# Kernel tuning notes

Measured on AMD Instinct MI355X. Metric: run time of the kernel, lower is better.

## Reference

```python
import jax, jax.numpy as jnp
import numpy as np

N_TOKENS = 100000
N_ARGS = 20000
N_EDGES = 320000
IN_DIM = 768
HEADS = 8
OUT_DIM = 64


def setup_inputs() -> dict:
    key = jax.random.key(0)
    k1, k2, k3, k4, k5 = jax.random.split(key, 5)
    h = jax.random.normal(k1, (N_TOKENS, IN_DIM), dtype=jnp.float32)
    W_fc = jax.random.normal(k2, (HEADS * OUT_DIM, IN_DIM), dtype=jnp.float32) * 0.05
    a_attn = jax.random.normal(k3, (2 * OUT_DIM,), dtype=jnp.float32) * 0.1
    edge_src = jax.random.randint(k4, (N_EDGES,), 0, N_TOKENS, dtype=jnp.int32)
    edge_dst = jax.random.randint(k5, (N_EDGES,), 0, N_ARGS, dtype=jnp.int32)
    return {"h": h, "W_fc": W_fc, "a_attn": a_attn,
            "edge_src": edge_src, "edge_dst": edge_dst}


def reference(h, W_fc, a_attn, edge_src, edge_dst):
    # z = fc(h) reshaped to [N_TOKENS, HEADS, OUT_DIM]
    z = (h @ W_fc.T).reshape(N_TOKENS, HEADS, OUT_DIM)
    # DGL zero-initializes 'z' on arg (dst) nodes, so the dst half of attn_fc
    # contributes 0; only the src half of the attention vector matters.
    a_src = a_attn[:OUT_DIM]
    s_node = jnp.einsum('nhd,d->nh', z, a_src)            # [N_TOKENS, H]
    e = jax.nn.leaky_relu(s_node[edge_src])               # [E, H]
    # segment softmax over incoming edges of each arg node
    m = jax.ops.segment_max(e, edge_dst, num_segments=N_ARGS)   # [N_ARGS, H]
    ex = jnp.exp(e - m[edge_dst])                          # [E, H]
    denom = jax.ops.segment_sum(ex, edge_dst, num_segments=N_ARGS)
    denom = jnp.where(denom == 0, 1.0, denom)
    alpha = ex / denom[edge_dst]                           # [E, H]
    # weighted neighbor aggregation
    msg = alpha[:, :, None] * z[edge_src]                  # [E, H, D]
    out = jax.ops.segment_sum(msg, edge_dst, num_segments=N_ARGS)  # [N_ARGS, H, D]
    return out
```

## Files before the change

kernel.cpp:

```cpp
#include <hip/hip_runtime.h>
#include <hip/hip_bf16.h>
#include <stdint.h>

#define N_TOKENS 100000
#define N_ARGS   20000
#define N_EDGES  320000
#define IN_DIM   768
#define HEADS    8
#define OUT_DIM  64
#define ZDIM     512

typedef unsigned short u16;
typedef unsigned int   u32;
typedef __bf16 bf16x8 __attribute__((ext_vector_type(8)));
typedef float  f32x4  __attribute__((ext_vector_type(4)));

__device__ __forceinline__ u16 f2bf(float f) {
    union { float f; u32 i; } v; v.f = f;
    u32 u = v.i;
    u += 0x7fffu + ((u >> 16) & 1u);
    return (u16)(u >> 16);
}
__device__ __forceinline__ float bf2f(u16 u) {
    union { u32 i; float f; } v; v.i = ((u32)u) << 16; return v.f;
}
__device__ __forceinline__ u32 pk(float lo, float hi) {
    __hip_bfloat162 r = __float22bfloat162_rn(float2{lo, hi});
    union { __hip_bfloat162 b; u32 u; } v; v.b = r; return v.u;
}
__device__ __forceinline__ uint4 pack8(const float4 p, const float4 q) {
    uint4 w;
    w.x = pk(p.x, p.y); w.y = pk(p.z, p.w);
    w.z = pk(q.x, q.y); w.w = pk(q.z, q.w);
    return w;
}

__global__ __launch_bounds__(256) void gemm_kernel(
    const float* __restrict__ A,
    const float* __restrict__ B,
    const float* __restrict__ a_attn,
    u16* __restrict__ z,
    float* __restrict__ s_node)
{
    __shared__ u16 As[128 * 32];
    __shared__ u16 Bs[128 * 32];

    const int tid  = threadIdx.x;
    const int wave = tid >> 6, lane = tid & 63;
    const int quad = lane >> 4, l16 = lane & 15;
    const int wm = wave >> 1, wn = wave & 1;
    const int bx = blockIdx.x;
    const int tileN = bx & 3;
    const int tileM = bx >> 2;

    const int tr = tid >> 1;
    const int tc = (tid & 1) * 16;
    int ga_row = tileM * 128 + tr; if (ga_row >= N_TOKENS) ga_row = N_TOKENS - 1;
    const float* gA = A + (size_t)ga_row * IN_DIM + tc;
    const float* gB = B + (size_t)(tileN * 128 + tr) * IN_DIM + tc;
    u16* sA = As + tid * 16;
    u16* sB = Bs + tid * 16;

    f32x4 acc[4][4];
    const f32x4 zero4 = {0.f, 0.f, 0.f, 0.f};
#pragma unroll
    for (int i = 0; i < 4; i++)
#pragma unroll
        for (int j = 0; j < 4; j++) acc[i][j] = zero4;

    for (int kt = 0; kt < IN_DIM / 32; ++kt) {
        const float4* pa = reinterpret_cast<const float4*>(gA + kt * 32);
        const float4* pb = reinterpret_cast<const float4*>(gB + kt * 32);
        const float4 a0 = pa[0], a1 = pa[1], a2 = pa[2], a3 = pa[3];
        const float4 b0 = pb[0], b1 = pb[1], b2 = pb[2], b3 = pb[3];
        __syncthreads();
        reinterpret_cast<uint4*>(sA)[0] = pack8(a0, a1);
        reinterpret_cast<uint4*>(sA)[1] = pack8(a2, a3);
        reinterpret_cast<uint4*>(sB)[0] = pack8(b0, b1);
        reinterpret_cast<uint4*>(sB)[1] = pack8(b2, b3);
        __syncthreads();

        bf16x8 aF[4], bF[4];
#pragma unroll
        for (int i = 0; i < 4; i++)
            aF[i] = *reinterpret_cast<const bf16x8*>(As + (wm * 64 + i * 16 + l16) * 32 + quad * 8);
#pragma unroll
        for (int j = 0; j < 4; j++)
            bF[j] = *reinterpret_cast<const bf16x8*>(Bs + (wn * 64 + j * 16 + l16) * 32 + quad * 8);
#pragma unroll
        for (int i = 0; i < 4; i++)
#pragma unroll
            for (int j = 0; j < 4; j++)
                acc[i][j] = __builtin_amdgcn_mfma_f32_16x16x32_bf16(aF[i], bF[j], acc[i][j], 0, 0, 0);
    }

    float av[4];
#pragma unroll
    for (int j = 0; j < 4; j++) av[j] = a_attn[j * 16 + l16];
    const int head = tileN * 2 + wn;
    const int colb = tileN * 128 + wn * 64;
#pragma unroll
    for (int i = 0; i < 4; i++) {
        const int rowb = tileM * 128 + wm * 64 + i * 16 + quad * 4;
#pragma unroll
        for (int r = 0; r < 4; r++) {
            const int row = rowb + r;
            const bool ok = row < N_TOKENS;
            float p = 0.0f;
#pragma unroll
            for (int j = 0; j < 4; j++) {
                const float v = acc[i][j][r];
                p += v * av[j];
                if (ok) z[(size_t)row * ZDIM + colb + j * 16 + l16] = f2bf(v);
            }
            p += __shfl_xor(p, 1);
            p += __shfl_xor(p, 2);
            p += __shfl_xor(p, 4);
            p += __shfl_xor(p, 8);
            if (ok && l16 == 0) s_node[row * HEADS + head] = p;
        }
    }
}

__global__ void zero_kernel(int* __restrict__ p, int n) {
    int i = blockIdx.x * blockDim.x + threadIdx.x;
    if (i < n) p[i] = 0;
}

__global__ void hist_kernel(const int* __restrict__ edst, int* __restrict__ counts) {
    int i = blockIdx.x * blockDim.x + threadIdx.x;
    if (i < N_EDGES) {
        int d = edst[i];
        if ((unsigned)d < (unsigned)N_ARGS) atomicAdd(&counts[d], 1);
    }
}

__global__ void scan_kernel(const int* __restrict__ counts, int* __restrict__ offsets,
                            int* __restrict__ cursor) {
    __shared__ int partial[1024];
    const int tid = threadIdx.x;
    const int C = 20;
    const int base = tid * C;
    int s = 0;
    for (int k = 0; k < C; k++) { int idx = base + k; if (idx < N_ARGS) s += counts[idx]; }
    partial[tid] = s;
    __syncthreads();
    for (int off = 1; off < 1024; off <<= 1) {
        int v = (tid >= off) ? partial[tid - off] : 0;
        __syncthreads();
        partial[tid] += v;
        __syncthreads();
    }
    int run = (tid == 0) ? 0 : partial[tid - 1];
    for (int k = 0; k < C; k++) {
        int idx = base + k;
        if (idx < N_ARGS) { offsets[idx] = run; cursor[idx] = run; run += counts[idx]; }
    }
    if (tid == 1023) offsets[N_ARGS] = run;
}

__global__ void scatter_kernel(const int* __restrict__ esrc, const int* __restrict__ edst,
                               int* __restrict__ cursor, int* __restrict__ ssrc) {
    int i = blockIdx.x * blockDim.x + threadIdx.x;
    if (i < N_EDGES) {
        int d = edst[i];
        if ((unsigned)d >= (unsigned)N_ARGS) return;
        int s = esrc[i];
        if ((unsigned)s >= (unsigned)N_TOKENS) s = 0;
        int pos = atomicAdd(&cursor[d], 1);
        ssrc[pos] = s;
    }
}

__global__ __launch_bounds__(256) void agg_kernel(
    const int* __restrict__ offsets, const int* __restrict__ sorted_src,
    const float* __restrict__ s_node, const u16* __restrict__ z,
    float* __restrict__ out)
{
    const int dst = blockIdx.x;
    const int tid = threadIdx.x;
    const int wave = tid >> 6, lane = tid & 63;
    const int start = offsets[dst];
    const int nE = offsets[dst + 1] - start;
    if (nE <= 0) {
        out[(size_t)dst * ZDIM + tid] = 0.0f;
        out[(size_t)dst * ZDIM + tid + 256] = 0.0f;
        return;
    }
    __shared__ float m8[8];
    __shared__ float inv8[8];
    __shared__ float scratch[32];
    __shared__ int   src_lds[64];
    __shared__ float alpha_lds[64 * 8];

    float lm[8];
#pragma unroll
    for (int h = 0; h < 8; h++) lm[h] = -1e30f;
    for (int j = tid; j < nE; j += 256) {
        int s = sorted_src[start + j];
        if ((unsigned)s >= (unsigned)N_TOKENS) s = 0;
#pragma unroll
        for (int h = 0; h < 8; h++) {
            float v = s_node[s * 8 + h];
            v = v > 0.0f ? v : 0.01f * v;
            lm[h] = fmaxf(lm[h], v);
        }
    }
#pragma unroll
    for (int off = 1; off < 64; off <<= 1)
#pragma unroll
        for (int h = 0; h < 8; h++) lm[h] = fmaxf(lm[h], __shfl_xor(lm[h], off));
    if (lane == 0) {
#pragma unroll
        for (int h = 0; h < 8; h++) scratch[wave * 8 + h] = lm[h];
    }
    __syncthreads();
    if (tid < 8) {
        float r = scratch[tid];
        for (int w = 1; w < 4; w++) r = fmaxf(r, scratch[w * 8 + tid]);
        m8[tid] = r;
    }
    __syncthreads();

    float ls[8];
#pragma unroll
    for (int h = 0; h < 8; h++) ls[h] = 0.0f;
    for (int j = tid; j < nE; j += 256) {
        int s = sorted_src[start + j];
        if ((unsigned)s >= (unsigned)N_TOKENS) s = 0;
#pragma unroll
        for (int h = 0; h < 8; h++) {
            float v = s_node[s * 8 + h];
            v = v > 0.0f ? v : 0.01f * v;
            ls[h] += __expf(v - m8[h]);
        }
    }
#pragma unroll
    for (int off = 1; off < 64; off <<= 1)
#pragma unroll
        for (int h = 0; h < 8; h++) ls[h] += __shfl_xor(ls[h], off);
    if (lane == 0) {
#pragma unroll
        for (int h = 0; h < 8; h++) scratch[wave * 8 + h] = ls[h];
    }
    __syncthreads();
    if (tid < 8) {
        float d = scratch[tid];
        for (int w = 1; w < 4; w++) d += scratch[w * 8 + tid];
        if (d == 0.0f) d = 1.0f;
        inv8[tid] = 1.0f / d;
    }
    __syncthreads();

    float acc0 = 0.0f, acc1 = 0.0f;
    const int h1 = tid >> 6;
    for (int c0 = 0; c0 < nE; c0 += 64) {
        const int cn = min(64, nE - c0);
        for (int j = tid; j < cn; j += 256) {
            int s = sorted_src[start + c0 + j];
            if ((unsigned)s >= (unsigned)N_TOKENS) s = 0;
            src_lds[j] = s;
        }
        __syncthreads();
        for (int idx = tid; idx < cn * 8; idx += 256) {
            const int j = idx >> 3, h = idx & 7;
            float v = s_node[src_lds[j] * 8 + h];
            v = v > 0.0f ? v : 0.01f * v;
            alpha_lds[idx] = __expf(v - m8[h]) * inv8[h];
        }
        __syncthreads();
        for (int j = 0; j < cn; j++) {
            const int row = src_lds[j];
            acc0 += alpha_lds[j * 8 + h1]     * bf2f(z[(size_t)row * ZDIM + tid]);
            acc1 += alpha_lds[j * 8 + h1 + 4] * bf2f(z[(size_t)row * ZDIM + 256 + tid]);
        }
        __syncthreads();
    }
    out[(size_t)dst * ZDIM + tid] = acc0;
    out[(size_t)dst * ZDIM + 256 + tid] = acc1;
}

extern "C" void kernel_launch(void* const* d_in, const int* in_sizes, int n_in,
                              void* d_out, int out_size, void* d_ws, size_t ws_size,
                              hipStream_t stream) {
    const float* h      = (const float*)d_in[0];
    const float* W      = (const float*)d_in[1];
    const float* a_attn = (const float*)d_in[2];
    const int* esrc     = (const int*)d_in[3];
    const int* edst     = (const int*)d_in[4];
    float* out          = (float*)d_out;

    char* ws = (char*)d_ws;
    u16*   z        = (u16*)ws;
    float* s_node   = (float*)(ws + 102400000);
    int*   counts   = (int*)(ws + 105600000);
    int*   offsets  = (int*)(ws + 105680000);
    int*   cursor   = (int*)(ws + 105760016);
    int*   ssrc     = (int*)(ws + 105840016);

    zero_kernel<<<(N_ARGS + 255) / 256, 256, 0, stream>>>(counts, N_ARGS);
    gemm_kernel<<<782 * 4, 256, 0, stream>>>(h, W, a_attn, z, s_node);
    hist_kernel<<<(N_EDGES + 255) / 256, 256, 0, stream>>>(edst, counts);
    scan_kernel<<<1, 1024, 0, stream>>>(counts, offsets, cursor);
    scatter_kernel<<<(N_EDGES + 255) / 256, 256, 0, stream>>>(esrc, edst, cursor, ssrc);
    agg_kernel<<<N_ARGS, 256, 0, stream>>>(offsets, ssrc, s_node, z, out);
}
```

Baseline: 777.4 us.

## Prefetch next k-tile into registers, swizzle LDS, and remap blocks across XCDs

The GEMM loop now issues the global loads for the next k-tile before the MFMA work on the current tile, so memory latency overlaps with compute. LDS writes and reads use an XOR swizzle on 16-byte chunks to reduce bank conflicts on the fragment reads. Block indices are remapped so that consecutive tiles land on the same XCD, which is meant to improve L2 reuse of the shared A rows. The prefetch adds register pressure, and the last iteration performs one redundant load.

```diff
diff --git a/kernel.cpp b/kernel.cpp
--- a/kernel.cpp
+++ b/kernel.cpp
@@ -49,17 +49,34 @@
     const int wave = tid >> 6, lane = tid & 63;
     const int quad = lane >> 4, l16 = lane & 15;
     const int wm = wave >> 1, wn = wave & 1;
+
     const int bx = blockIdx.x;
-    const int tileN = bx & 3;
-    const int tileM = bx >> 2;
+    const int lb = (bx & 7) * 391 + (bx >> 3);
+    const int tileN = lb & 3;
+    const int tileM = lb >> 2;
 
     const int tr = tid >> 1;
     const int tc = (tid & 1) * 16;
     int ga_row = tileM * 128 + tr; if (ga_row >= N_TOKENS) ga_row = N_TOKENS - 1;
     const float* gA = A + (size_t)ga_row * IN_DIM + tc;
     const float* gB = B + (size_t)(tileN * 128 + tr) * IN_DIM + tc;
-    u16* sA = As + tid * 16;
-    u16* sB = Bs + tid * 16;
+
+    const int swr = (tr >> 1) & 3;
+    const int s0  = (tid & 1) * 2;
+    u16* sA0 = As + tr * 32 + (((s0    ) ^ swr) * 8);
+    u16* sA1 = As + tr * 32 + (((s0 + 1) ^ swr) * 8);
+    u16* sB0 = Bs + tr * 32 + (((s0    ) ^ swr) * 8);
+    u16* sB1 = Bs + tr * 32 + (((s0 + 1) ^ swr) * 8);
+
+    const u16* rA[4];
+    const u16* rB[4];
+#pragma unroll
+    for (int i = 0; i < 4; i++) {
+        int r = wm * 64 + i * 16 + l16;
+        rA[i] = As + r * 32 + (((quad ^ ((r >> 1) & 3))) * 8);
+        r = wn * 64 + i * 16 + l16;
+        rB[i] = Bs + r * 32 + (((quad ^ ((r >> 1) & 3))) * 8);
+    }
 
     f32x4 acc[4][4];
     const f32x4 zero4 = {0.f, 0.f, 0.f, 0.f};
@@ -68,30 +85,43 @@
 #pragma unroll
         for (int j = 0; j < 4; j++) acc[i][j] = zero4;
 
+    float4 a0, a1, a2, a3, b0, b1, b2, b3;
+    {
+        const float4* pa = reinterpret_cast<const float4*>(gA);
+        const float4* pb = reinterpret_cast<const float4*>(gB);
+        a0 = pa[0]; a1 = pa[1]; a2 = pa[2]; a3 = pa[3];
+        b0 = pb[0]; b1 = pb[1]; b2 = pb[2]; b3 = pb[3];
+    }
+
     for (int kt = 0; kt < IN_DIM / 32; ++kt) {
-        const float4* pa = reinterpret_cast<const float4*>(gA + kt * 32);
-        const float4* pb = reinterpret_cast<const float4*>(gB + kt * 32);
-        const float4 a0 = pa[0], a1 = pa[1], a2 = pa[2], a3 = pa[3];
-        const float4 b0 = pb[0], b1 = pb[1], b2 = pb[2], b3 = pb[3];
-        __syncthreads();
-        reinterpret_cast<uint4*>(sA)[0] = pack8(a0, a1);
-        reinterpret_cast<uint4*>(sA)[1] = pack8(a2, a3);
-        reinterpret_cast<uint4*>(sB)[0] = pack8(b0, b1);
-        reinterpret_cast<uint4*>(sB)[1] = pack8(b2, b3);
-        __syncthreads();
+        __syncthreads();
+        reinterpret_cast<uint4*>(sA0)[0] = pack8(a0, a1);
+        reinterpret_cast<uint4*>(sA1)[0] = pack8(a2, a3);
+        reinterpret_cast<uint4*>(sB0)[0] = pack8(b0, b1);
+        reinterpret_cast<uint4*>(sB1)[0] = pack8(b2, b3);
+        __syncthreads();
+
+        {
+            const int kn = (kt < IN_DIM / 32 - 1) ? kt + 1 : kt;
+            const float4* pa = reinterpret_cast<const float4*>(gA + kn * 32);
+            const float4* pb = reinterpret_cast<const float4*>(gB + kn * 32);
+            a0 = pa[0]; a1 = pa[1]; a2 = pa[2]; a3 = pa[3];
+            b0 = pb[0]; b1 = pb[1]; b2 = pb[2]; b3 = pb[3];
+        }
 
         bf16x8 aF[4], bF[4];
 #pragma unroll
         for (int i = 0; i < 4; i++)
-            aF[i] = *reinterpret_cast<const bf16x8*>(As + (wm * 64 + i * 16 + l16) * 32 + quad * 8);
+            aF[i] = *reinterpret_cast<const bf16x8*>(rA[i]);
 #pragma unroll
         for (int j = 0; j < 4; j++)
-            bF[j] = *reinterpret_cast<const bf16x8*>(Bs + (wn * 64 + j * 16 + l16) * 32 + quad * 8);
+            bF[j] = *reinterpret_cast<const bf16x8*>(rB[j]);
 #pragma unroll
         for (int i = 0; i < 4; i++)
 #pragma unroll
             for (int j = 0; j < 4; j++)
                 acc[i][j] = __builtin_amdgcn_mfma_f32_16x16x32_bf16(aF[i], bF[j], acc[i][j], 0, 0, 0);
+
     }
 
     float av[4];
```

Result: no change. 788.6 us (+1.4%).

## Use direct global-to-LDS loads with swizzled layout and pre-converted bf16 weights

Applied to the files above, without the earlier changes.

Pre-converts W to bf16 in a separate small kernel, then loads A (fp32) and B (bf16) tiles straight into LDS with global_load_lds. A uses an XOR-swizzled layout and is converted to bf16 when read back from LDS. Block indices are also remapped across groups of 8 to change how tiles are spread. The aim is to drop the register round-trip and packing on the load path and to cut LDS bank conflicts. In exchange, A now takes twice the LDS space as fp32, there is still no double buffering, and one extra kernel launch is added.

```diff
diff --git a/kernel.cpp b/kernel.cpp
--- a/kernel.cpp
+++ b/kernel.cpp
@@ -34,32 +34,77 @@
     w.z = pk(q.x, q.y); w.w = pk(q.z, q.w);
     return w;
 }
+__device__ __forceinline__ void load_lds16(const void* g, void* l) {
+    __builtin_amdgcn_global_load_lds(
+        (const __attribute__((address_space(1))) void*)g,
+        (__attribute__((address_space(3))) void*)l, 16, 0, 0);
+}
+
+__global__ __launch_bounds__(256) void convert_w(const float* __restrict__ W,
+                                                 u16* __restrict__ Wbf) {
+    const int i = blockIdx.x * blockDim.x + threadIdx.x;
+    if (i < ZDIM * IN_DIM / 8) {
+        const float4* p = reinterpret_cast<const float4*>(W + (size_t)i * 8);
+        const float4 x = p[0], y = p[1];
+        reinterpret_cast<uint4*>(Wbf)[i] = pack8(x, y);
+    }
+}
 
 __global__ __launch_bounds__(256) void gemm_kernel(
     const float* __restrict__ A,
-    const float* __restrict__ B,
+    const u16*   __restrict__ Bbf,
     const float* __restrict__ a_attn,
     u16* __restrict__ z,
     float* __restrict__ s_node)
 {
-    __shared__ u16 As[128 * 32];
-    __shared__ u16 Bs[128 * 32];
+    __shared__ float As[128 * 32];
+    __shared__ u16   Bs[128 * 32];
 
     const int tid  = threadIdx.x;
     const int wave = tid >> 6, lane = tid & 63;
     const int quad = lane >> 4, l16 = lane & 15;
     const int wm = wave >> 1, wn = wave & 1;
+
     const int bx = blockIdx.x;
-    const int tileN = bx & 3;
-    const int tileM = bx >> 2;
-
-    const int tr = tid >> 1;
-    const int tc = (tid & 1) * 16;
-    int ga_row = tileM * 128 + tr; if (ga_row >= N_TOKENS) ga_row = N_TOKENS - 1;
-    const float* gA = A + (size_t)ga_row * IN_DIM + tc;
-    const float* gB = B + (size_t)(tileN * 128 + tr) * IN_DIM + tc;
-    u16* sA = As + tid * 16;
-    u16* sB = Bs + tid * 16;
+    const int lb = (bx & 7) * 391 + (bx >> 3);
+    const int tileN = lb & 3;
+    const int tileM = lb >> 2;
+
+    const char* srcA[4];
+    void*       dstA[4];
+#pragma unroll
+    for (int g = 0; g < 4; g++) {
+        const int idx = (wave * 4 + g) * 64 + lane;
+        const int row = idx >> 3, s = idx & 7;
+        const int c = s ^ (row & 7);
+        int grow = tileM * 128 + row;
+        if (grow >= N_TOKENS) grow = N_TOKENS - 1;
+        srcA[g] = (const char*)(A + (size_t)grow * IN_DIM + c * 4);
+        dstA[g] = (char*)As + (size_t)(wave * 4 + g) * 1024;
+    }
+    const char* srcB[2];
+    void*       dstB[2];
+#pragma unroll
+    for (int g = 0; g < 2; g++) {
+        const int idx = (wave * 2 + g) * 64 + lane;
+        const int row = idx >> 2, s = idx & 3;
+        const int c = s ^ ((row >> 1) & 3);
+        srcB[g] = (const char*)(Bbf + (size_t)(tileN * 128 + row) * IN_DIM + c * 8);
+        dstB[g] = (char*)Bs + (size_t)(wave * 2 + g) * 1024;
+    }
+
+    const float* rA0[4];
+    const float* rA1[4];
+    const u16*   rB[4];
+#pragma unroll
+    for (int i = 0; i < 4; i++) {
+        int r = wm * 64 + i * 16 + l16;
+        const int sl = (quad * 2) ^ (r & 7);
+        rA0[i] = As + r * 32 + sl * 4;
+        rA1[i] = As + r * 32 + (sl ^ 1) * 4;
+        r = wn * 64 + i * 16 + l16;
+        rB[i] = Bs + r * 32 + ((quad ^ ((r >> 1) & 3)) * 8);
+    }
 
     f32x4 acc[4][4];
     const f32x4 zero4 = {0.f, 0.f, 0.f, 0.f};
@@ -69,29 +114,35 @@
         for (int j = 0; j < 4; j++) acc[i][j] = zero4;
 
     for (int kt = 0; kt < IN_DIM / 32; ++kt) {
-        const float4* pa = reinterpret_cast<const float4*>(gA + kt * 32);
-        const float4* pb = reinterpret_cast<const float4*>(gB + kt * 32);
-        const float4 a0 = pa[0], a1 = pa[1], a2 = pa[2], a3 = pa[3];
-        const float4 b0 = pb[0], b1 = pb[1], b2 = pb[2], b3 = pb[3];
-        __syncthreads();
-        reinterpret_cast<uint4*>(sA)[0] = pack8(a0, a1);
-        reinterpret_cast<uint4*>(sA)[1] = pack8(a2, a3);
-        reinterpret_cast<uint4*>(sB)[0] = pack8(b0, b1);
-        reinterpret_cast<uint4*>(sB)[1] = pack8(b2, b3);
+        __syncthreads();
+#pragma unroll
+        for (int g = 0; g < 4; g++) load_lds16(srcA[g], dstA[g]);
+#pragma unroll
+        for (int g = 0; g < 2; g++) load_lds16(srcB[g], dstB[g]);
         __syncthreads();
 
         bf16x8 aF[4], bF[4];
 #pragma unroll
-        for (int i = 0; i < 4; i++)
-            aF[i] = *reinterpret_cast<const bf16x8*>(As + (wm * 64 + i * 16 + l16) * 32 + quad * 8);
+        for (int i = 0; i < 4; i++) {
+            const float4 lo = *reinterpret_cast<const float4*>(rA0[i]);
+            const float4 hi = *reinterpret_cast<const float4*>(rA1[i]);
+            union { uint4 u; bf16x8 b; } cv;
+            cv.u = pack8(lo, hi);
+            aF[i] = cv.b;
+        }
 #pragma unroll
         for (int j = 0; j < 4; j++)
-            bF[j] = *reinterpret_cast<const bf16x8*>(Bs + (wn * 64 + j * 16 + l16) * 32 + quad * 8);
+            bF[j] = *reinterpret_cast<const bf16x8*>(rB[j]);
 #pragma unroll
         for (int i = 0; i < 4; i++)
 #pragma unroll
             for (int j = 0; j < 4; j++)
                 acc[i][j] = __builtin_amdgcn_mfma_f32_16x16x32_bf16(aF[i], bF[j], acc[i][j], 0, 0, 0);
+
+#pragma unroll
+        for (int g = 0; g < 4; g++) srcA[g] += 128;
+#pragma unroll
+        for (int g = 0; g < 2; g++) srcB[g] += 64;
     }
 
     float av[4];
@@ -297,9 +348,11 @@
     int*   offsets  = (int*)(ws + 105680000);
     int*   cursor   = (int*)(ws + 105760016);
     int*   ssrc     = (int*)(ws + 105840016);
+    u16*   wbf      = (u16*)(ws + 107120016);
 
     zero_kernel<<<(N_ARGS + 255) / 256, 256, 0, stream>>>(counts, N_ARGS);
-    gemm_kernel<<<782 * 4, 256, 0, stream>>>(h, W, a_attn, z, s_node);
+    convert_w<<<(ZDIM * IN_DIM / 8 + 255) / 256, 256, 0, stream>>>(W, wbf);
+    gemm_kernel<<<782 * 4, 256, 0, stream>>>(h, wbf, a_attn, z, s_node);
     hist_kernel<<<(N_EDGES + 255) / 256, 256, 0, stream>>>(edst, counts);
     scan_kernel<<<1, 1024, 0, stream>>>(counts, offsets, cursor);
     scatter_kernel<<<(N_EDGES + 255) / 256, 256, 0, stream>>>(esrc, edst, cursor, ssrc);
```

Measured after the change: 717.7 us. -7.7%, faster.
